# Performance work log

Measured on AMD Instinct MI355X. Metric: run time of the kernel, lower is better.

Reference implementation:

```python
import jax, jax.numpy as jnp
from jax import lax
import numpy as np

NUM_KIND = 4
V, H, B = 34, 32, 4096   # raw vertical (2 rows dropped), horizontal, batch
KS = 33                  # odd-rounded max(V-2, H)
NUM_DEPTH = 4
N_SQ = 100


def _conv(x, w):
    # x: (N,1,h,w), w: (1,1,KS,KS); torch Conv2d == cross-correlation == lax default
    return lax.conv_general_dilated(x, w, (1, 1), 'SAME',
                                    dimension_numbers=('NCHW', 'OIHW', 'NCHW'))


def _conv_k(x, w):
    # x: (K,B,1,h,w) -> conv each map with the shared 1-channel kernel
    k, b, c, h, wd = x.shape
    return _conv(x.reshape(k * b, c, h, wd), w).reshape(k, b, c, h, wd)


def setup_inputs() -> dict:
    key = jax.random.key(0)
    ks = jax.random.split(key, 8)
    std = 0.3
    return {
        'dots':    jax.random.randint(ks[0], (V, H, B), 0, NUM_KIND + 1, dtype=jnp.int32),
        'w_each':  jax.random.normal(ks[1], (1, 1, KS, KS), jnp.float32) * std,
        'w_not':   jax.random.normal(ks[2], (1, 1, KS, KS), jnp.float32) * std,
        'w_not2':  jax.random.normal(ks[3], (1, 1, KS, KS), jnp.float32) * std,
        'w_empty': jax.random.normal(ks[4], (1, 1, KS, KS), jnp.float32) * std,
        'W1':      jax.random.normal(ks[5], (N_SQ, (V - 2) * H), jnp.float32) * std,
        'W2':      jax.random.normal(ks[6], (N_SQ, N_SQ), jnp.float32) * std,
        'W3':      jax.random.normal(ks[7], (1, N_SQ), jnp.float32) * std,
    }


def reference(dots, w_each, w_not, w_not2, w_empty, W1, W2, W3):
    # drop last 2 vertical rows, layout (V-2,H,B) -> (B,1,V-2,H)
    board = dots[:-2].astype(jnp.float32).transpose(2, 0, 1)[:, None]  # (B,1,h,w)

    empty = (board == 0).astype(jnp.float32)
    E = _conv(empty, w_empty)                                           # (B,1,h,w)

    kinds = jnp.arange(1, NUM_KIND + 1, dtype=board.dtype).reshape(NUM_KIND, 1, 1, 1, 1)
    each = (board[None] == kinds).astype(jnp.float32)                   # (K,B,1,h,w)
    notm = ((each + empty[None]) == 0).astype(jnp.float32)              # (K,B,1,h,w)

    # first pass: per-color value, masked to that color's cells
    notm_conv = _conv_k(notm, w_not)      # note: the torch code LOGS the convolved not-mask
    v = _conv_k(each, w_each) + E[None] - notm_conv
    L = each * v                          # each_color_value_log (masked)
    s = jax.nn.sigmoid(L.sum(axis=0))     # all_color_value_2nd, (B,1,h,w)

    # iterative diffusion; torch mutates the log in-place each depth:
    # L <- mask * (L + E + conv2nd(notm_conv * before)); before is detached
    for _ in range(NUM_DEPTH):
        before = lax.stop_gradient(s)
        C = _conv_k(notm_conv * before[None], w_not2)
        L = each * (L + E[None] + C)
        s = jax.nn.sigmoid(L.sum(axis=0))

    feat = s.reshape(s.shape[0], -1)      # (B, (V-2)*H)
    x = jax.nn.leaky_relu(feat @ W1.T, 0.2)
    x = jax.nn.leaky_relu(x @ W2.T, 0.2)
    return x @ W3.T                        # (B,1)
```

## Files before the change

### kernel.cpp

```cpp
#include <hip/hip_runtime.h>
#include <cstdint>
#include <cstddef>


typedef _Float16 f16;
typedef __attribute__((ext_vector_type(8))) _Float16 f16x8;
typedef __attribute__((ext_vector_type(4))) float f32x4;

#define NB   4096
#define PIX  1024
#define MR   (NB * 4)

__device__ __forceinline__ void gld_lds16(const void* g, void* l) {
    __builtin_amdgcn_global_load_lds(
        (const __attribute__((address_space(1))) void*)g,
        (__attribute__((address_space(3))) void*)l, 16, 0, 0);
}

__global__ void build_mats(const float* __restrict__ we, const float* __restrict__ wn,
                           const float* __restrict__ wn2, const float* __restrict__ wem,
                           f16* __restrict__ Mn, f16* __restrict__ Mn2,
                           f16* __restrict__ Mem, f16* __restrict__ Bst) {
    int idx = blockIdx.x * 256 + threadIdx.x;
    int o = idx >> 10, in = idx & 1023;
    int i = o >> 5, j = o & 31, a = in >> 5, b = in & 31;
    int u = a - i + 16, v = b - j + 16;
    bool ok = (u >= 0) && (u < 33) && (v >= 0) && (v < 33);
    int w = u * 33 + v;
    float ve = 0.f, vn = 0.f, vn2 = 0.f, vem = 0.f;
    if (ok) { ve = we[w]; vn = wn[w]; vn2 = wn2[w]; vem = wem[w]; }
    Mn[idx]  = (f16)vn;
    Mn2[idx] = (f16)vn2;
    Mem[idx] = (f16)vem;
    Bst[(size_t)o * 2048 + in]        = (f16)(ve + vn);
    Bst[(size_t)o * 2048 + 1024 + in] = (f16)(vem + vn);
}

__global__ void tn_build(const f16* __restrict__ Mn, float* __restrict__ tn) {
    int o = blockIdx.x * 256 + threadIdx.x;
    float s = 0.f;
    for (int j = 0; j < 128; j++) {
        f16x8 v = *(const f16x8*)(Mn + (size_t)o * 1024 + j * 8);
#pragma unroll
        for (int e = 0; e < 8; e++) s += (float)v[e];
    }
    tn[o] = s;
}

__global__ void build_w1(const float* __restrict__ W1, f16* __restrict__ W1b) {
    int idx = blockIdx.x * 256 + threadIdx.x;
    int j = idx >> 10, i = idx & 1023;
    W1b[idx] = (f16)(j < 100 ? W1[j * 1024 + i] : 0.f);
}

__global__ void build_board(const int* __restrict__ dots, unsigned char* __restrict__ board) {
    __shared__ unsigned char tile[64][68];
    int t = threadIdx.x;
    int bp = blockIdx.x & 15, bn = blockIdx.x >> 4;
    int p0 = bp * 64, n0 = bn * 64;
    int ln = t & 63, lp = t >> 6;
#pragma unroll
    for (int j = 0; j < 16; j++) {
        int p = lp * 16 + j;
        tile[p][ln] = (unsigned char)dots[(size_t)(p0 + p) * 4096 + n0 + ln];
    }
    __syncthreads();
#pragma unroll
    for (int j = 0; j < 16; j++) {
        int n = lp * 16 + j;
        board[(size_t)(n0 + n) * 1024 + p0 + ln] = tile[ln][n];
    }
}

template <int MODE, int ASRC>
__device__ __forceinline__ void run_gemm(
    int bjob, int ypx, int nx, char* smem,
    const f16* __restrict__ X, const f16* __restrict__ B, int K,
    const unsigned char* __restrict__ board, const f16* __restrict__ NCs,
    const f16* __restrict__ Sin, const f16* __restrict__ En,
    const float* __restrict__ tn, float* __restrict__ Lsel,
    f16* __restrict__ outB, int ldo, float* __restrict__ outF) {
    char* smB = smem;
    char* smA = smem + 16384;
    char* smS = smem + 32768;

    const int tid = threadIdx.x;
    const int wv = tid >> 6, ln = tid & 63;
    const int wm = wv >> 1, wn_ = wv & 1;
    const int lr = ln & 15, lq = ln >> 4;

    int xcd = bjob & 7, slot = bjob >> 3;
    int bx = slot % nx;
    int by = xcd * ypx + slot / nx;
    const int rtile = by * 128, otile = bx * 128;
    const int img0 = (ASRC == 4) ? rtile : (rtile >> 2);

    const f32x4 fz = {0.f, 0.f, 0.f, 0.f};
    f32x4 acc[4][4];
#pragma unroll
    for (int i = 0; i < 4; i++)
#pragma unroll
        for (int j = 0; j < 4; j++) acc[i][j] = fz;

    for (int kb = 0; kb < K; kb += 64) {
#pragma unroll
        for (int t = 0; t < 4; t++) {
            int c = t * 256 + wv * 64 + ln;
            int row = c >> 3, gcol = (c & 7) ^ (row & 7);
            gld_lds16(B + (size_t)(otile + row) * K + kb + gcol * 8, smB + c * 16);
        }
        if (ASRC == 0) {
#pragma unroll
            for (int t = 0; t < 4; t++) {
                int c = t * 256 + wv * 64 + ln;
                int row = c >> 3, gcol = (c & 7) ^ (row & 7);
                gld_lds16(X + (size_t)(rtile + row) * K + kb + gcol * 8, smA + c * 16);
            }
        } else if (ASRC == 1) {
#pragma unroll
            for (int t = 0; t < 4; t++) {
                int c = t * 256 + wv * 64 + ln;
                int row = c >> 3, gcol = (c & 7) ^ (row & 7);
                gld_lds16(NCs + (size_t)(rtile + row) * 1024 + kb + gcol * 8, smA + c * 16);
            }
            {
                int c = wv * 64 + ln;
                int row = c >> 3, gcol = (c & 7) ^ (row & 7);
                gld_lds16(Sin + (size_t)(img0 + row) * 1024 + kb + gcol * 8, smS + c * 16);
            }
        } else if (ASRC == 4) {
            int cb = kb;
#pragma unroll
            for (int t = 0; t < 2; t++) {
                int c = t * 256 + wv * 64 + ln;
                int row = c >> 2, g = (c & 3) ^ (row & 3);
                gld_lds16(board + (size_t)(img0 + row) * 1024 + cb + g * 16, smA + c * 16);
            }
        } else {
            int cb = (ASRC == 5) ? (kb & 1023) : kb;
            if (wv < 2) {
                int c = wv * 64 + ln;
                int row = c >> 2, g = (c & 3) ^ (row & 3);
                gld_lds16(board + (size_t)(img0 + row) * 1024 + cb + g * 16, smA + c * 16);
            }
        }
        __syncthreads();

#pragma unroll
        for (int kk = 0; kk < 2; kk++) {
            const int oct = kk * 4 + lq;
            f16x8 af[4], bfr[4];
#pragma unroll
            for (int i = 0; i < 4; i++) {
                int rrow = wm * 64 + i * 16 + lr;
                if (ASRC == 0) {
                    af[i] = *(const f16x8*)(smA + rrow * 128 + (oct ^ (rrow & 7)) * 16);
                } else if (ASRC == 1) {
                    f16x8 nc = *(const f16x8*)(smA + rrow * 128 + (oct ^ (rrow & 7)) * 16);
                    int img = rrow >> 2;
                    f16x8 sv = *(const f16x8*)(smS + img * 128 + (oct ^ (img & 7)) * 16);
                    af[i] = nc * sv;
                } else {
                    int m = (ASRC == 4) ? rrow : (rrow >> 2);
                    int k1 = (rrow & 3) + 1;
                    uint64_t bb = *(const uint64_t*)(smA + m * 64 +
                                    (((oct >> 1)) ^ (m & 3)) * 16 + (oct & 1) * 8);
                    bool ext = (ASRC == 5) && (kb >= 1024);
                    f16x8 v;
#pragma unroll
                    for (int jj = 0; jj < 8; jj++) {
                        int bj = (int)((bb >> (8 * jj)) & 0xff);
                        bool on = (ASRC == 4) ? (bj == 0)
                                : (ASRC == 3) ? (bj != 0 && bj != k1)
                                : ext          ? (bj == 0)
                                               : (bj == k1);
                        v[jj] = on ? (f16)1.f : (f16)0.f;
                    }
                    af[i] = v;
                }
            }
#pragma unroll
            for (int j = 0; j < 4; j++) {
                int brow = wn_ * 64 + j * 16 + lr;
                bfr[j] = *(const f16x8*)(smB + brow * 128 + (oct ^ (brow & 7)) * 16);
            }
#pragma unroll
            for (int i = 0; i < 4; i++)
#pragma unroll
                for (int j = 0; j < 4; j++)
                    acc[i][j] = __builtin_amdgcn_mfma_f32_16x16x32_f16(
                        af[i], bfr[j], acc[i][j], 0, 0, 0);
        }
        __syncthreads();
    }

#pragma unroll
    for (int i = 0; i < 4; i++) {
        int rbase = rtile + wm * 64 + i * 16 + lq * 4;
#pragma unroll
        for (int j = 0; j < 4; j++) {
            int o = otile + wn_ * 64 + j * 16 + lr;
            f32x4 a = acc[i][j];
            if (MODE == 0) {
#pragma unroll
                for (int v = 0; v < 4; v++)
                    outB[(size_t)(rbase + v) * ldo + o] = (f16)a[v];
            } else if (MODE == 5) {
#pragma unroll
                for (int v = 0; v < 4; v++) {
                    float x = a[v];
                    outF[(size_t)(rbase + v) * ldo + o] = x > 0.f ? x : 0.2f * x;
                }
            } else {
                int n = rbase >> 2;
                size_t no = (size_t)n * PIX + o;
                int c = board[no];
                float asel = (c == 1) ? a[0] : (c == 2) ? a[1] : (c == 3) ? a[2] : a[3];
                float Lnew;
                if (MODE == 2) {
                    Lnew = (c > 0) ? (asel - tn[o]) : 0.f;
                } else {
                    float E = (float)En[no];
                    Lnew = (c > 0) ? (Lsel[no] + E + asel) : 0.f;
                }
                float s = 1.f / (1.f + __expf(-Lnew));
                if (MODE != 4) Lsel[no] = Lnew;
                outB[no] = (f16)s;
            }
        }
    }
}

__global__ void __launch_bounds__(256, 4) gemm_fa(
    const f16* __restrict__ Bst, const f16* __restrict__ Mn,
    const f16* __restrict__ Mem, const unsigned char* __restrict__ board,
    const float* __restrict__ tn, float* __restrict__ Lsel,
    f16* __restrict__ Sa, f16* __restrict__ NC, f16* __restrict__ En) {
    __shared__ __attribute__((aligned(16))) char smem[24576];
    int bi = blockIdx.x;
    if (bi < 1024) {
        run_gemm<2, 5>(bi, 16, 8, smem, nullptr, Bst, 2048, board, nullptr,
                       nullptr, nullptr, tn, Lsel, Sa, 0, nullptr);
    } else if (bi < 2048) {
        run_gemm<0, 3>(bi - 1024, 16, 8, smem, nullptr, Mn, 1024, board, nullptr,
                       nullptr, nullptr, nullptr, nullptr, NC, PIX, nullptr);
    } else {
        run_gemm<0, 4>(bi - 2048, 4, 8, smem, nullptr, Mem, 1024, board, nullptr,
                       nullptr, nullptr, nullptr, nullptr, En, PIX, nullptr);
    }
}

template <int MODE>
__global__ void __launch_bounds__(256, 4) gemm_depth(
    const f16* __restrict__ Mn2, const unsigned char* __restrict__ board,
    const f16* __restrict__ NCs, const f16* __restrict__ Sin,
    const f16* __restrict__ En, float* __restrict__ Lsel,
    f16* __restrict__ outB) {
    __shared__ __attribute__((aligned(16))) char smem[36864];
    run_gemm<MODE, 1>(blockIdx.x, 16, 8, smem, nullptr, Mn2, 1024, board, NCs,
                      Sin, En, nullptr, Lsel, outB, 0, nullptr);
}

__global__ void __launch_bounds__(256, 4) gemm_mlp(
    const f16* __restrict__ feat, const f16* __restrict__ W1b,
    float* __restrict__ X1) {
    __shared__ __attribute__((aligned(16))) char smem[32768];
    run_gemm<5, 0>(blockIdx.x, 4, 1, smem, feat, W1b, 1024, nullptr, nullptr,
                   nullptr, nullptr, nullptr, nullptr, nullptr, 128, X1);
}

__global__ void __launch_bounds__(256) mlp23(const float* __restrict__ X1,
                                             const float* __restrict__ W2,
                                             const float* __restrict__ W3,
                                             float* __restrict__ out) {
    __shared__ float sW2[10000];
    __shared__ float sW3[100];
    __shared__ float red[256];
    int t = threadIdx.x;
    for (int idx = t; idx < 10000; idx += 256) sW2[idx] = W2[idx];
    if (t < 100) sW3[t] = W3[t];
    __syncthreads();
    int nb = t >> 2, q = t & 3;
    int n = blockIdx.x * 64 + nb;
    const float* x1 = X1 + (size_t)n * 128;
    float xr[100];
#pragma unroll
    for (int i = 0; i < 100; i++) xr[i] = x1[i];
    float partial = 0.f;
    for (int jj = 0; jj < 25; jj++) {
        int j = q + jj * 4;
        const float* w2r = sW2 + j * 100;
        float acc2 = 0.f;
#pragma unroll
        for (int i = 0; i < 100; i++) acc2 += w2r[i] * xr[i];
        partial += sW3[j] * (acc2 > 0.f ? acc2 : 0.2f * acc2);
    }
    red[t] = partial;
    __syncthreads();
    if (q == 0) out[n] = red[t] + red[t + 1] + red[t + 2] + red[t + 3];
}

extern "C" void kernel_launch(void* const* d_in, const int* in_sizes, int n_in,
                              void* d_out, int out_size, void* d_ws, size_t ws_size,
                              hipStream_t stream) {
    (void)in_sizes; (void)n_in; (void)out_size; (void)ws_size;
    const int*   dots   = (const int*)d_in[0];
    const float* w_each = (const float*)d_in[1];
    const float* w_not  = (const float*)d_in[2];
    const float* w_not2 = (const float*)d_in[3];
    const float* w_emp  = (const float*)d_in[4];
    const float* W1 = (const float*)d_in[5];
    const float* W2 = (const float*)d_in[6];
    const float* W3 = (const float*)d_in[7];
    float* out = (float*)d_out;

    char* ws = (char*)d_ws;
    size_t off = 0;
    auto alloc = [&](size_t bytes) -> char* {
        char* p = ws + off;
        off += (bytes + 255) & ~(size_t)255;
        return p;
    };
    f16* Mn   = (f16*)alloc((size_t)PIX * PIX * 2);
    f16* Mn2  = (f16*)alloc((size_t)PIX * PIX * 2);
    f16* Mem  = (f16*)alloc((size_t)PIX * PIX * 2);
    f16* Bst  = (f16*)alloc((size_t)PIX * 2048 * 2);
    f16* W1b  = (f16*)alloc((size_t)128 * PIX * 2);
    unsigned char* board = (unsigned char*)alloc((size_t)NB * PIX);
    f16*   NC   = (f16*)alloc((size_t)MR * PIX * 2);
    f16*   En   = (f16*)alloc((size_t)NB * PIX * 2);
    f16*   Sa   = (f16*)alloc((size_t)NB * PIX * 2);
    f16*   Sb   = (f16*)alloc((size_t)NB * PIX * 2);
    f16*   feat = (f16*)alloc((size_t)NB * PIX * 2);
    float* Lsel = (float*)alloc((size_t)NB * PIX * 4);
    float* tn   = (float*)alloc((size_t)PIX * 4);
    float* X1   = (float*)alloc((size_t)NB * 128 * 4);

    build_mats<<<4096, 256, 0, stream>>>(w_each, w_not, w_not2, w_emp, Mn, Mn2, Mem, Bst);
    tn_build<<<4, 256, 0, stream>>>(Mn, tn);
    build_w1<<<512, 256, 0, stream>>>(W1, W1b);
    build_board<<<1024, 256, 0, stream>>>(dots, board);

    dim3 blk(256);
    gemm_fa<<<2304, blk, 0, stream>>>(Bst, Mn, Mem, board, tn, Lsel, Sa, NC, En);
    gemm_depth<3><<<1024, blk, 0, stream>>>(Mn2, board, NC, Sa, En, Lsel, Sb);
    gemm_depth<3><<<1024, blk, 0, stream>>>(Mn2, board, NC, Sb, En, Lsel, Sa);
    gemm_depth<3><<<1024, blk, 0, stream>>>(Mn2, board, NC, Sa, En, Lsel, Sb);
    gemm_depth<4><<<1024, blk, 0, stream>>>(Mn2, board, NC, Sb, En, Lsel, feat);
    gemm_mlp<<<32, blk, 0, stream>>>(feat, W1b, X1);
    mlp23<<<64, blk, 0, stream>>>(X1, W2, W3, out);
}
```

Measured before the change: 433.1 us.

## Precompute f16 mask matrices, widen GEMM N-tile to 256, split first-pass GEMMs

A new kernel materializes the per-kind, not-mask and empty-mask indicator matrices in f16 up front, so the GEMMs load them directly instead of decoding board bytes into masks inside the inner loop. The first-pass stacked GEMM (K=2048) is split into separate K=1024 GEMMs: the E and E-plus-not-conv products are stacked along N, and the sigmoid/Lsel init moves into a new elementwise kernel. GEMM tiles become 128x256 with 3 blocks per CU, halving the depth-grid size and reusing each A tile across more outputs. The cost is several large extra mask buffers, more global traffic for the materialized masks, and an extra elementwise pass.

```diff
diff --git a/kernel.cpp b/kernel.cpp
--- a/kernel.cpp
+++ b/kernel.cpp
@@ -20,7 +20,7 @@
 __global__ void build_mats(const float* __restrict__ we, const float* __restrict__ wn,
                            const float* __restrict__ wn2, const float* __restrict__ wem,
                            f16* __restrict__ Mn, f16* __restrict__ Mn2,
-                           f16* __restrict__ Mem, f16* __restrict__ Bst) {
+                           f16* __restrict__ BstS1, f16* __restrict__ BstE) {
     int idx = blockIdx.x * 256 + threadIdx.x;
     int o = idx >> 10, in = idx & 1023;
     int i = o >> 5, j = o & 31, a = in >> 5, b = in & 31;
@@ -29,11 +29,11 @@
     int w = u * 33 + v;
     float ve = 0.f, vn = 0.f, vn2 = 0.f, vem = 0.f;
     if (ok) { ve = we[w]; vn = wn[w]; vn2 = wn2[w]; vem = wem[w]; }
-    Mn[idx]  = (f16)vn;
-    Mn2[idx] = (f16)vn2;
-    Mem[idx] = (f16)vem;
-    Bst[(size_t)o * 2048 + in]        = (f16)(ve + vn);
-    Bst[(size_t)o * 2048 + 1024 + in] = (f16)(vem + vn);
+    Mn[idx]    = (f16)vn;
+    Mn2[idx]   = (f16)vn2;
+    BstS1[idx] = (f16)(ve + vn);
+    BstE[idx]                          = (f16)vem;
+    BstE[(size_t)(1024 + o) * 1024 + in] = (f16)(vem + vn);
 }
 
 __global__ void tn_build(const f16* __restrict__ Mn, float* __restrict__ tn) {
@@ -72,17 +72,43 @@
     }
 }
 
-template <int MODE, int ASRC>
+__global__ void build_masks(const unsigned char* __restrict__ board,
+                            f16* __restrict__ Xe, f16* __restrict__ Xn,
+                            f16* __restrict__ Xz) {
+    int idx = blockIdx.x * 256 + threadIdx.x;
+    int n = idx >> 10, p = idx & 1023;
+    int c = board[idx];
+    Xz[idx] = (f16)(c == 0 ? 1.f : 0.f);
+    size_t base = (size_t)n * 4096 + p;
+#pragma unroll
+    for (int k = 0; k < 4; k++) {
+        Xe[base + k * 1024] = (f16)((c == k + 1) ? 1.f : 0.f);
+        Xn[base + k * 1024] = (f16)((c != 0 && c != k + 1) ? 1.f : 0.f);
+    }
+}
+
+__global__ void mk_sa(const f16* __restrict__ S1sel, const f16* __restrict__ EplusM,
+                      const unsigned char* __restrict__ board,
+                      float* __restrict__ Lsel, f16* __restrict__ Sa) {
+    int idx = blockIdx.x * 256 + threadIdx.x;
+    int c = board[idx];
+    float L = (c > 0) ? ((float)S1sel[idx] + (float)EplusM[idx]) : 0.f;
+    Lsel[idx] = L;
+    Sa[idx] = (f16)(1.f / (1.f + __expf(-L)));
+}
+
+template <int MODE, int ASRC, int NTJ>
 __device__ __forceinline__ void run_gemm(
     int bjob, int ypx, int nx, char* smem,
-    const f16* __restrict__ X, const f16* __restrict__ B, int K,
+    const f16* __restrict__ X, const f16* __restrict__ B,
     const unsigned char* __restrict__ board, const f16* __restrict__ NCs,
     const f16* __restrict__ Sin, const f16* __restrict__ En,
     const float* __restrict__ tn, float* __restrict__ Lsel,
     f16* __restrict__ outB, int ldo, float* __restrict__ outF) {
+    constexpr int BN = NTJ * 32;
     char* smB = smem;
-    char* smA = smem + 16384;
-    char* smS = smem + 32768;
+    char* smA = smem + BN * 128;
+    char* smS = smA + 16384;
 
     const int tid = threadIdx.x;
     const int wv = tid >> 6, ln = tid & 63;
@@ -92,104 +118,62 @@
     int xcd = bjob & 7, slot = bjob >> 3;
     int bx = slot % nx;
     int by = xcd * ypx + slot / nx;
-    const int rtile = by * 128, otile = bx * 128;
-    const int img0 = (ASRC == 4) ? rtile : (rtile >> 2);
+    const int rtile = by * 128, otile = bx * BN;
+    const int img0 = rtile >> 2;
 
     const f32x4 fz = {0.f, 0.f, 0.f, 0.f};
-    f32x4 acc[4][4];
+    f32x4 acc[4][NTJ];
 #pragma unroll
     for (int i = 0; i < 4; i++)
 #pragma unroll
-        for (int j = 0; j < 4; j++) acc[i][j] = fz;
-
-    for (int kb = 0; kb < K; kb += 64) {
+        for (int j = 0; j < NTJ; j++) acc[i][j] = fz;
+
+    for (int kb = 0; kb < 1024; kb += 64) {
+#pragma unroll
+        for (int t = 0; t < NTJ; t++) {
+            int c = t * 256 + wv * 64 + ln;
+            int row = c >> 3, gcol = (c & 7) ^ (row & 7);
+            gld_lds16(B + (size_t)(otile + row) * 1024 + kb + gcol * 8, smB + c * 16);
+        }
 #pragma unroll
         for (int t = 0; t < 4; t++) {
             int c = t * 256 + wv * 64 + ln;
             int row = c >> 3, gcol = (c & 7) ^ (row & 7);
-            gld_lds16(B + (size_t)(otile + row) * K + kb + gcol * 8, smB + c * 16);
-        }
-        if (ASRC == 0) {
-#pragma unroll
-            for (int t = 0; t < 4; t++) {
-                int c = t * 256 + wv * 64 + ln;
-                int row = c >> 3, gcol = (c & 7) ^ (row & 7);
-                gld_lds16(X + (size_t)(rtile + row) * K + kb + gcol * 8, smA + c * 16);
-            }
-        } else if (ASRC == 1) {
-#pragma unroll
-            for (int t = 0; t < 4; t++) {
-                int c = t * 256 + wv * 64 + ln;
-                int row = c >> 3, gcol = (c & 7) ^ (row & 7);
-                gld_lds16(NCs + (size_t)(rtile + row) * 1024 + kb + gcol * 8, smA + c * 16);
-            }
-            {
-                int c = wv * 64 + ln;
-                int row = c >> 3, gcol = (c & 7) ^ (row & 7);
-                gld_lds16(Sin + (size_t)(img0 + row) * 1024 + kb + gcol * 8, smS + c * 16);
-            }
-        } else if (ASRC == 4) {
-            int cb = kb;
-#pragma unroll
-            for (int t = 0; t < 2; t++) {
-                int c = t * 256 + wv * 64 + ln;
-                int row = c >> 2, g = (c & 3) ^ (row & 3);
-                gld_lds16(board + (size_t)(img0 + row) * 1024 + cb + g * 16, smA + c * 16);
-            }
-        } else {
-            int cb = (ASRC == 5) ? (kb & 1023) : kb;
-            if (wv < 2) {
-                int c = wv * 64 + ln;
-                int row = c >> 2, g = (c & 3) ^ (row & 3);
-                gld_lds16(board + (size_t)(img0 + row) * 1024 + cb + g * 16, smA + c * 16);
-            }
+            const f16* src = (ASRC == 0) ? X : NCs;
+            gld_lds16(src + (size_t)(rtile + row) * 1024 + kb + gcol * 8, smA + c * 16);
+        }
+        if (ASRC == 1) {
+            int c = wv * 64 + ln;
+            int row = c >> 3, gcol = (c & 7) ^ (row & 7);
+            gld_lds16(Sin + (size_t)(img0 + row) * 1024 + kb + gcol * 8, smS + c * 16);
         }
         __syncthreads();
 
 #pragma unroll
         for (int kk = 0; kk < 2; kk++) {
             const int oct = kk * 4 + lq;
-            f16x8 af[4], bfr[4];
+            f16x8 af[4];
 #pragma unroll
             for (int i = 0; i < 4; i++) {
                 int rrow = wm * 64 + i * 16 + lr;
                 if (ASRC == 0) {
                     af[i] = *(const f16x8*)(smA + rrow * 128 + (oct ^ (rrow & 7)) * 16);
-                } else if (ASRC == 1) {
+                } else {
                     f16x8 nc = *(const f16x8*)(smA + rrow * 128 + (oct ^ (rrow & 7)) * 16);
                     int img = rrow >> 2;
                     f16x8 sv = *(const f16x8*)(smS + img * 128 + (oct ^ (img & 7)) * 16);
                     af[i] = nc * sv;
-                } else {
-                    int m = (ASRC == 4) ? rrow : (rrow >> 2);
-                    int k1 = (rrow & 3) + 1;
-                    uint64_t bb = *(const uint64_t*)(smA + m * 64 +
-                                    (((oct >> 1)) ^ (m & 3)) * 16 + (oct & 1) * 8);
-                    bool ext = (ASRC == 5) && (kb >= 1024);
-                    f16x8 v;
-#pragma unroll
-                    for (int jj = 0; jj < 8; jj++) {
-                        int bj = (int)((bb >> (8 * jj)) & 0xff);
-                        bool on = (ASRC == 4) ? (bj == 0)
-                                : (ASRC == 3) ? (bj != 0 && bj != k1)
-                                : ext          ? (bj == 0)
-                                               : (bj == k1);
-                        v[jj] = on ? (f16)1.f : (f16)0.f;
-                    }
-                    af[i] = v;
                 }
             }
 #pragma unroll
-            for (int j = 0; j < 4; j++) {
-                int brow = wn_ * 64 + j * 16 + lr;
-                bfr[j] = *(const f16x8*)(smB + brow * 128 + (oct ^ (brow & 7)) * 16);
+            for (int j = 0; j < NTJ; j++) {
+                int brow = wn_ * (NTJ * 16) + j * 16 + lr;
+                f16x8 bf = *(const f16x8*)(smB + brow * 128 + (oct ^ (brow & 7)) * 16);
+#pragma unroll
+                for (int i = 0; i < 4; i++)
+                    acc[i][j] = __builtin_amdgcn_mfma_f32_16x16x32_f16(
+                        af[i], bf, acc[i][j], 0, 0, 0);
             }
-#pragma unroll
-            for (int i = 0; i < 4; i++)
-#pragma unroll
-                for (int j = 0; j < 4; j++)
-                    acc[i][j] = __builtin_amdgcn_mfma_f32_16x16x32_f16(
-                        af[i], bfr[j], acc[i][j], 0, 0, 0);
         }
         __syncthreads();
     }
@@ -198,13 +182,23 @@
     for (int i = 0; i < 4; i++) {
         int rbase = rtile + wm * 64 + i * 16 + lq * 4;
 #pragma unroll
-        for (int j = 0; j < 4; j++) {
-            int o = otile + wn_ * 64 + j * 16 + lr;
+        for (int j = 0; j < NTJ; j++) {
+            int o = otile + wn_ * (NTJ * 16) + j * 16 + lr;
             f32x4 a = acc[i][j];
             if (MODE == 0) {
 #pragma unroll
                 for (int v = 0; v < 4; v++)
                     outB[(size_t)(rbase + v) * ldo + o] = (f16)a[v];
+            } else if (MODE == 2) {
+#pragma unroll
+                for (int v = 0; v < 4; v++) {
+                    int n = rbase + v;
+                    if (o < 1024)
+                        outB[(size_t)n * 1024 + o] = (f16)a[v];
+                    else
+                        outB[(size_t)(NB + n) * 1024 + (o - 1024)] =
+                            (f16)(a[v] - tn[o - 1024]);
+                }
             } else if (MODE == 5) {
 #pragma unroll
                 for (int v = 0; v < 4; v++) {
@@ -216,57 +210,57 @@
                 size_t no = (size_t)n * PIX + o;
                 int c = board[no];
                 float asel = (c == 1) ? a[0] : (c == 2) ? a[1] : (c == 3) ? a[2] : a[3];
-                float Lnew;
-                if (MODE == 2) {
-                    Lnew = (c > 0) ? (asel - tn[o]) : 0.f;
+                if (MODE == 1) {
+                    outB[no] = (f16)asel;
                 } else {
                     float E = (float)En[no];
-                    Lnew = (c > 0) ? (Lsel[no] + E + asel) : 0.f;
+                    float Lnew = (c > 0) ? (Lsel[no] + E + asel) : 0.f;
+                    float s = 1.f / (1.f + __expf(-Lnew));
+                    if (MODE != 4) Lsel[no] = Lnew;
+                    outB[no] = (f16)s;
                 }
-                float s = 1.f / (1.f + __expf(-Lnew));
-                if (MODE != 4) Lsel[no] = Lnew;
-                outB[no] = (f16)s;
             }
         }
     }
 }
 
-__global__ void __launch_bounds__(256, 4) gemm_fa(
-    const f16* __restrict__ Bst, const f16* __restrict__ Mn,
-    const f16* __restrict__ Mem, const unsigned char* __restrict__ board,
-    const float* __restrict__ tn, float* __restrict__ Lsel,
-    f16* __restrict__ Sa, f16* __restrict__ NC, f16* __restrict__ En) {
-    __shared__ __attribute__((aligned(16))) char smem[24576];
+__global__ void __launch_bounds__(256, 3) gemm_fa(
+    const f16* __restrict__ Xe, const f16* __restrict__ Xn,
+    const f16* __restrict__ Xz, const f16* __restrict__ BstS1,
+    const f16* __restrict__ Mn, const f16* __restrict__ BstE,
+    const unsigned char* __restrict__ board, const float* __restrict__ tn,
+    f16* __restrict__ S1sel, f16* __restrict__ NC, f16* __restrict__ EnBoth) {
+    __shared__ __attribute__((aligned(16))) char smem[49152];
     int bi = blockIdx.x;
-    if (bi < 1024) {
-        run_gemm<2, 5>(bi, 16, 8, smem, nullptr, Bst, 2048, board, nullptr,
-                       nullptr, nullptr, tn, Lsel, Sa, 0, nullptr);
-    } else if (bi < 2048) {
-        run_gemm<0, 3>(bi - 1024, 16, 8, smem, nullptr, Mn, 1024, board, nullptr,
-                       nullptr, nullptr, nullptr, nullptr, NC, PIX, nullptr);
+    if (bi < 512) {
+        run_gemm<1, 0, 8>(bi, 16, 4, smem, Xe, BstS1, board, nullptr, nullptr,
+                          nullptr, nullptr, nullptr, S1sel, 0, nullptr);
+    } else if (bi < 1024) {
+        run_gemm<0, 0, 8>(bi - 512, 16, 4, smem, Xn, Mn, nullptr, nullptr, nullptr,
+                          nullptr, nullptr, nullptr, NC, PIX, nullptr);
     } else {
-        run_gemm<0, 4>(bi - 2048, 4, 8, smem, nullptr, Mem, 1024, board, nullptr,
-                       nullptr, nullptr, nullptr, nullptr, En, PIX, nullptr);
+        run_gemm<2, 0, 8>(bi - 1024, 4, 8, smem, Xz, BstE, nullptr, nullptr, nullptr,
+                          nullptr, tn, nullptr, EnBoth, 0, nullptr);
     }
 }
 
 template <int MODE>
-__global__ void __launch_bounds__(256, 4) gemm_depth(
+__global__ void __launch_bounds__(256, 3) gemm_depth(
     const f16* __restrict__ Mn2, const unsigned char* __restrict__ board,
     const f16* __restrict__ NCs, const f16* __restrict__ Sin,
     const f16* __restrict__ En, float* __restrict__ Lsel,
     f16* __restrict__ outB) {
-    __shared__ __attribute__((aligned(16))) char smem[36864];
-    run_gemm<MODE, 1>(blockIdx.x, 16, 8, smem, nullptr, Mn2, 1024, board, NCs,
-                      Sin, En, nullptr, Lsel, outB, 0, nullptr);
-}
-
-__global__ void __launch_bounds__(256, 4) gemm_mlp(
+    __shared__ __attribute__((aligned(16))) char smem[53248];
+    run_gemm<MODE, 1, 8>(blockIdx.x, 16, 4, smem, nullptr, Mn2, board, NCs,
+                         Sin, En, nullptr, Lsel, outB, 0, nullptr);
+}
+
+__global__ void __launch_bounds__(256, 3) gemm_mlp(
     const f16* __restrict__ feat, const f16* __restrict__ W1b,
     float* __restrict__ X1) {
     __shared__ __attribute__((aligned(16))) char smem[32768];
-    run_gemm<5, 0>(blockIdx.x, 4, 1, smem, feat, W1b, 1024, nullptr, nullptr,
-                   nullptr, nullptr, nullptr, nullptr, nullptr, 128, X1);
+    run_gemm<5, 0, 4>(blockIdx.x, 4, 1, smem, feat, W1b, nullptr, nullptr,
+                      nullptr, nullptr, nullptr, nullptr, nullptr, 128, X1);
 }
 
 __global__ void __launch_bounds__(256) mlp23(const float* __restrict__ X1,
@@ -321,32 +315,42 @@
         off += (bytes + 255) & ~(size_t)255;
         return p;
     };
-    f16* Mn   = (f16*)alloc((size_t)PIX * PIX * 2);
-    f16* Mn2  = (f16*)alloc((size_t)PIX * PIX * 2);
-    f16* Mem  = (f16*)alloc((size_t)PIX * PIX * 2);
-    f16* Bst  = (f16*)alloc((size_t)PIX * 2048 * 2);
-    f16* W1b  = (f16*)alloc((size_t)128 * PIX * 2);
+    f16* Mn    = (f16*)alloc((size_t)PIX * PIX * 2);
+    f16* Mn2   = (f16*)alloc((size_t)PIX * PIX * 2);
+    f16* BstS1 = (f16*)alloc((size_t)PIX * PIX * 2);
+    f16* BstE  = (f16*)alloc((size_t)2048 * PIX * 2);
+    f16* W1b   = (f16*)alloc((size_t)128 * PIX * 2);
     unsigned char* board = (unsigned char*)alloc((size_t)NB * PIX);
-    f16*   NC   = (f16*)alloc((size_t)MR * PIX * 2);
-    f16*   En   = (f16*)alloc((size_t)NB * PIX * 2);
-    f16*   Sa   = (f16*)alloc((size_t)NB * PIX * 2);
-    f16*   Sb   = (f16*)alloc((size_t)NB * PIX * 2);
-    f16*   feat = (f16*)alloc((size_t)NB * PIX * 2);
-    float* Lsel = (float*)alloc((size_t)NB * PIX * 4);
-    float* tn   = (float*)alloc((size_t)PIX * 4);
-    float* X1   = (float*)alloc((size_t)NB * 128 * 4);
-
-    build_mats<<<4096, 256, 0, stream>>>(w_each, w_not, w_not2, w_emp, Mn, Mn2, Mem, Bst);
+    f16* Xe    = (f16*)alloc((size_t)MR * PIX * 2);
+    f16* Xn    = (f16*)alloc((size_t)MR * PIX * 2);
+    f16* Xz    = (f16*)alloc((size_t)NB * PIX * 2);
+    f16* NC    = (f16*)alloc((size_t)MR * PIX * 2);
+    f16* EnBoth= (f16*)alloc((size_t)2 * NB * PIX * 2);
+    f16* S1sel = (f16*)alloc((size_t)NB * PIX * 2);
+    f16* Sa    = (f16*)alloc((size_t)NB * PIX * 2);
+    f16* Sb    = (f16*)alloc((size_t)NB * PIX * 2);
+    f16* feat  = (f16*)alloc((size_t)NB * PIX * 2);
+    float* Lsel= (float*)alloc((size_t)NB * PIX * 4);
+    float* tn  = (float*)alloc((size_t)PIX * 4);
+    float* X1  = (float*)alloc((size_t)NB * 128 * 4);
+
+    build_board<<<1024, 256, 0, stream>>>(dots, board);
+    build_mats<<<4096, 256, 0, stream>>>(w_each, w_not, w_not2, w_emp,
+                                         Mn, Mn2, BstS1, BstE);
     tn_build<<<4, 256, 0, stream>>>(Mn, tn);
     build_w1<<<512, 256, 0, stream>>>(W1, W1b);
-    build_board<<<1024, 256, 0, stream>>>(dots, board);
+    build_masks<<<16384, 256, 0, stream>>>(board, Xe, Xn, Xz);
 
     dim3 blk(256);
-    gemm_fa<<<2304, blk, 0, stream>>>(Bst, Mn, Mem, board, tn, Lsel, Sa, NC, En);
-    gemm_depth<3><<<1024, blk, 0, stream>>>(Mn2, board, NC, Sa, En, Lsel, Sb);
-    gemm_depth<3><<<1024, blk, 0, stream>>>(Mn2, board, NC, Sb, En, Lsel, Sa);
-    gemm_depth<3><<<1024, blk, 0, stream>>>(Mn2, board, NC, Sa, En, Lsel, Sb);
-    gemm_depth<4><<<1024, blk, 0, stream>>>(Mn2, board, NC, Sb, En, Lsel, feat);
+    gemm_fa<<<1280, blk, 0, stream>>>(Xe, Xn, Xz, BstS1, Mn, BstE, board, tn,
+                                      S1sel, NC, EnBoth);
+    f16* En = EnBoth;
+    f16* EplusM = EnBoth + (size_t)NB * PIX;
+    mk_sa<<<16384, blk, 0, stream>>>(S1sel, EplusM, board, Lsel, Sa);
+    gemm_depth<3><<<512, blk, 0, stream>>>(Mn2, board, NC, Sa, En, Lsel, Sb);
+    gemm_depth<3><<<512, blk, 0, stream>>>(Mn2, board, NC, Sb, En, Lsel, Sa);
+    gemm_depth<3><<<512, blk, 0, stream>>>(Mn2, board, NC, Sa, En, Lsel, Sb);
+    gemm_depth<4><<<512, blk, 0, stream>>>(Mn2, board, NC, Sb, En, Lsel, feat);
     gemm_mlp<<<32, blk, 0, stream>>>(feat, W1b, X1);
     mlp23<<<64, blk, 0, stream>>>(X1, W2, W3, out);
 }
```

Result: slower. 755.1 us (+74.3%).

## Split first-pass GEMM, add elementwise sigmoid kernel, prefuse NC*S into LDS

Applied to the files above, without the earlier changes.

Replaces the stacked K=2048 first-pass GEMM (each+not and empty+not weights, with a tn correction) by a plain K=1024 GEMM on Me. A new elementwise kernel then combines the result with the already computed En and NC to form L and the first sigmoid. The depth GEMMs now multiply NC by S in registers before writing to LDS, instead of staging S separately and multiplying after each LDS read. The LDS load mapping is also reordered per wave. This removes K work and the tn kernel, but adds an extra launch and an extra full pass over NC, En and L, and it drops async global-to-LDS loads for the depth A operand.

```diff
diff --git a/kernel.cpp b/kernel.cpp
--- a/kernel.cpp
+++ b/kernel.cpp
@@ -19,8 +19,8 @@
 
 __global__ void build_mats(const float* __restrict__ we, const float* __restrict__ wn,
                            const float* __restrict__ wn2, const float* __restrict__ wem,
-                           f16* __restrict__ Mn, f16* __restrict__ Mn2,
-                           f16* __restrict__ Mem, f16* __restrict__ Bst) {
+                           f16* __restrict__ Me, f16* __restrict__ Mn,
+                           f16* __restrict__ Mn2, f16* __restrict__ Mem) {
     int idx = blockIdx.x * 256 + threadIdx.x;
     int o = idx >> 10, in = idx & 1023;
     int i = o >> 5, j = o & 31, a = in >> 5, b = in & 31;
@@ -29,22 +29,10 @@
     int w = u * 33 + v;
     float ve = 0.f, vn = 0.f, vn2 = 0.f, vem = 0.f;
     if (ok) { ve = we[w]; vn = wn[w]; vn2 = wn2[w]; vem = wem[w]; }
+    Me[idx]  = (f16)ve;
     Mn[idx]  = (f16)vn;
     Mn2[idx] = (f16)vn2;
     Mem[idx] = (f16)vem;
-    Bst[(size_t)o * 2048 + in]        = (f16)(ve + vn);
-    Bst[(size_t)o * 2048 + 1024 + in] = (f16)(vem + vn);
-}
-
-__global__ void tn_build(const f16* __restrict__ Mn, float* __restrict__ tn) {
-    int o = blockIdx.x * 256 + threadIdx.x;
-    float s = 0.f;
-    for (int j = 0; j < 128; j++) {
-        f16x8 v = *(const f16x8*)(Mn + (size_t)o * 1024 + j * 8);
-#pragma unroll
-        for (int e = 0; e < 8; e++) s += (float)v[e];
-    }
-    tn[o] = s;
 }
 
 __global__ void build_w1(const float* __restrict__ W1, f16* __restrict__ W1b) {
@@ -72,17 +60,32 @@
     }
 }
 
+__global__ void mk_sa(const f16* __restrict__ S1sel, const f16* __restrict__ En,
+                      const f16* __restrict__ NC,
+                      const unsigned char* __restrict__ board,
+                      float* __restrict__ Lsel, f16* __restrict__ Sa) {
+    int idx = blockIdx.x * 256 + threadIdx.x;
+    int n = idx >> 10, o = idx & 1023;
+    int c = board[idx];
+    float L = 0.f;
+    if (c > 0) {
+        float ncsel = (float)NC[(size_t)(4 * n + c - 1) * 1024 + o];
+        L = (float)S1sel[idx] + (float)En[idx] - ncsel;
+    }
+    Lsel[idx] = L;
+    Sa[idx] = (f16)(1.f / (1.f + __expf(-L)));
+}
+
 template <int MODE, int ASRC>
 __device__ __forceinline__ void run_gemm(
     int bjob, int ypx, int nx, char* smem,
-    const f16* __restrict__ X, const f16* __restrict__ B, int K,
+    const f16* __restrict__ X, const f16* __restrict__ B,
     const unsigned char* __restrict__ board, const f16* __restrict__ NCs,
     const f16* __restrict__ Sin, const f16* __restrict__ En,
-    const float* __restrict__ tn, float* __restrict__ Lsel,
-    f16* __restrict__ outB, int ldo, float* __restrict__ outF) {
+    float* __restrict__ Lsel, f16* __restrict__ outB, int ldo,
+    float* __restrict__ outF) {
     char* smB = smem;
     char* smA = smem + 16384;
-    char* smS = smem + 32768;
 
     const int tid = threadIdx.x;
     const int wv = tid >> 6, ln = tid & 63;
@@ -102,46 +105,42 @@
 #pragma unroll
         for (int j = 0; j < 4; j++) acc[i][j] = fz;
 
-    for (int kb = 0; kb < K; kb += 64) {
+    for (int kb = 0; kb < 1024; kb += 64) {
 #pragma unroll
         for (int t = 0; t < 4; t++) {
-            int c = t * 256 + wv * 64 + ln;
+            int c = (wv * 4 + t) * 64 + ln;
             int row = c >> 3, gcol = (c & 7) ^ (row & 7);
-            gld_lds16(B + (size_t)(otile + row) * K + kb + gcol * 8, smB + c * 16);
+            gld_lds16(B + (size_t)(otile + row) * 1024 + kb + gcol * 8, smB + c * 16);
         }
         if (ASRC == 0) {
 #pragma unroll
             for (int t = 0; t < 4; t++) {
-                int c = t * 256 + wv * 64 + ln;
+                int c = (wv * 4 + t) * 64 + ln;
                 int row = c >> 3, gcol = (c & 7) ^ (row & 7);
-                gld_lds16(X + (size_t)(rtile + row) * K + kb + gcol * 8, smA + c * 16);
+                gld_lds16(X + (size_t)(rtile + row) * 1024 + kb + gcol * 8, smA + c * 16);
             }
         } else if (ASRC == 1) {
 #pragma unroll
             for (int t = 0; t < 4; t++) {
-                int c = t * 256 + wv * 64 + ln;
+                int c = (wv * 4 + t) * 64 + ln;
                 int row = c >> 3, gcol = (c & 7) ^ (row & 7);
-                gld_lds16(NCs + (size_t)(rtile + row) * 1024 + kb + gcol * 8, smA + c * 16);
-            }
-            {
-                int c = wv * 64 + ln;
-                int row = c >> 3, gcol = (c & 7) ^ (row & 7);
-                gld_lds16(Sin + (size_t)(img0 + row) * 1024 + kb + gcol * 8, smS + c * 16);
+                int gr = rtile + row;
+                f16x8 nc = *(const f16x8*)(NCs + (size_t)gr * 1024 + kb + gcol * 8);
+                f16x8 sv = *(const f16x8*)(Sin + (size_t)(gr >> 2) * 1024 + kb + gcol * 8);
+                *(f16x8*)(smA + c * 16) = nc * sv;
             }
         } else if (ASRC == 4) {
-            int cb = kb;
 #pragma unroll
             for (int t = 0; t < 2; t++) {
                 int c = t * 256 + wv * 64 + ln;
                 int row = c >> 2, g = (c & 3) ^ (row & 3);
-                gld_lds16(board + (size_t)(img0 + row) * 1024 + cb + g * 16, smA + c * 16);
+                gld_lds16(board + (size_t)(img0 + row) * 1024 + kb + g * 16, smA + c * 16);
             }
         } else {
-            int cb = (ASRC == 5) ? (kb & 1023) : kb;
             if (wv < 2) {
                 int c = wv * 64 + ln;
                 int row = c >> 2, g = (c & 3) ^ (row & 3);
-                gld_lds16(board + (size_t)(img0 + row) * 1024 + cb + g * 16, smA + c * 16);
+                gld_lds16(board + (size_t)(img0 + row) * 1024 + kb + g * 16, smA + c * 16);
             }
         }
         __syncthreads();
@@ -153,27 +152,20 @@
 #pragma unroll
             for (int i = 0; i < 4; i++) {
                 int rrow = wm * 64 + i * 16 + lr;
-                if (ASRC == 0) {
+                if (ASRC == 0 || ASRC == 1) {
                     af[i] = *(const f16x8*)(smA + rrow * 128 + (oct ^ (rrow & 7)) * 16);
-                } else if (ASRC == 1) {
-                    f16x8 nc = *(const f16x8*)(smA + rrow * 128 + (oct ^ (rrow & 7)) * 16);
-                    int img = rrow >> 2;
-                    f16x8 sv = *(const f16x8*)(smS + img * 128 + (oct ^ (img & 7)) * 16);
-                    af[i] = nc * sv;
                 } else {
                     int m = (ASRC == 4) ? rrow : (rrow >> 2);
                     int k1 = (rrow & 3) + 1;
                     uint64_t bb = *(const uint64_t*)(smA + m * 64 +
-                                    (((oct >> 1)) ^ (m & 3)) * 16 + (oct & 1) * 8);
-                    bool ext = (ASRC == 5) && (kb >= 1024);
+                                    ((oct >> 1) ^ (m & 3)) * 16 + (oct & 1) * 8);
                     f16x8 v;
 #pragma unroll
                     for (int jj = 0; jj < 8; jj++) {
                         int bj = (int)((bb >> (8 * jj)) & 0xff);
-                        bool on = (ASRC == 4) ? (bj == 0)
+                        bool on = (ASRC == 2) ? (bj == k1)
                                 : (ASRC == 3) ? (bj != 0 && bj != k1)
-                                : ext          ? (bj == 0)
-                                               : (bj == k1);
+                                              : (bj == 0);
                         v[jj] = on ? (f16)1.f : (f16)0.f;
                     }
                     af[i] = v;
@@ -216,37 +208,35 @@
                 size_t no = (size_t)n * PIX + o;
                 int c = board[no];
                 float asel = (c == 1) ? a[0] : (c == 2) ? a[1] : (c == 3) ? a[2] : a[3];
-                float Lnew;
-                if (MODE == 2) {
-                    Lnew = (c > 0) ? (asel - tn[o]) : 0.f;
+                if (MODE == 1) {
+                    outB[no] = (f16)asel;
                 } else {
                     float E = (float)En[no];
-                    Lnew = (c > 0) ? (Lsel[no] + E + asel) : 0.f;
+                    float Lnew = (c > 0) ? (Lsel[no] + E + asel) : 0.f;
+                    float s = 1.f / (1.f + __expf(-Lnew));
+                    if (MODE != 4) Lsel[no] = Lnew;
+                    outB[no] = (f16)s;
                 }
-                float s = 1.f / (1.f + __expf(-Lnew));
-                if (MODE != 4) Lsel[no] = Lnew;
-                outB[no] = (f16)s;
             }
         }
     }
 }
 
 __global__ void __launch_bounds__(256, 4) gemm_fa(
-    const f16* __restrict__ Bst, const f16* __restrict__ Mn,
+    const f16* __restrict__ Me, const f16* __restrict__ Mn,
     const f16* __restrict__ Mem, const unsigned char* __restrict__ board,
-    const float* __restrict__ tn, float* __restrict__ Lsel,
-    f16* __restrict__ Sa, f16* __restrict__ NC, f16* __restrict__ En) {
+    f16* __restrict__ S1sel, f16* __restrict__ NC, f16* __restrict__ En) {
     __shared__ __attribute__((aligned(16))) char smem[24576];
     int bi = blockIdx.x;
     if (bi < 1024) {
-        run_gemm<2, 5>(bi, 16, 8, smem, nullptr, Bst, 2048, board, nullptr,
-                       nullptr, nullptr, tn, Lsel, Sa, 0, nullptr);
+        run_gemm<1, 2>(bi, 16, 8, smem, nullptr, Me, board, nullptr, nullptr,
+                       nullptr, nullptr, S1sel, 0, nullptr);
     } else if (bi < 2048) {
-        run_gemm<0, 3>(bi - 1024, 16, 8, smem, nullptr, Mn, 1024, board, nullptr,
-                       nullptr, nullptr, nullptr, nullptr, NC, PIX, nullptr);
+        run_gemm<0, 3>(bi - 1024, 16, 8, smem, nullptr, Mn, board, nullptr, nullptr,
+                       nullptr, nullptr, NC, PIX, nullptr);
     } else {
-        run_gemm<0, 4>(bi - 2048, 4, 8, smem, nullptr, Mem, 1024, board, nullptr,
-                       nullptr, nullptr, nullptr, nullptr, En, PIX, nullptr);
+        run_gemm<0, 4>(bi - 2048, 4, 8, smem, nullptr, Mem, board, nullptr, nullptr,
+                       nullptr, nullptr, En, PIX, nullptr);
     }
 }
 
@@ -256,17 +246,17 @@
     const f16* __restrict__ NCs, const f16* __restrict__ Sin,
     const f16* __restrict__ En, float* __restrict__ Lsel,
     f16* __restrict__ outB) {
-    __shared__ __attribute__((aligned(16))) char smem[36864];
-    run_gemm<MODE, 1>(blockIdx.x, 16, 8, smem, nullptr, Mn2, 1024, board, NCs,
-                      Sin, En, nullptr, Lsel, outB, 0, nullptr);
+    __shared__ __attribute__((aligned(16))) char smem[32768];
+    run_gemm<MODE, 1>(blockIdx.x, 16, 8, smem, nullptr, Mn2, board, NCs,
+                      Sin, En, Lsel, outB, 0, nullptr);
 }
 
 __global__ void __launch_bounds__(256, 4) gemm_mlp(
     const f16* __restrict__ feat, const f16* __restrict__ W1b,
     float* __restrict__ X1) {
     __shared__ __attribute__((aligned(16))) char smem[32768];
-    run_gemm<5, 0>(blockIdx.x, 4, 1, smem, feat, W1b, 1024, nullptr, nullptr,
-                   nullptr, nullptr, nullptr, nullptr, nullptr, 128, X1);
+    run_gemm<5, 0>(blockIdx.x, 4, 1, smem, feat, W1b, nullptr, nullptr,
+                   nullptr, nullptr, nullptr, nullptr, 128, X1);
 }
 
 __global__ void __launch_bounds__(256) mlp23(const float* __restrict__ X1,
@@ -321,28 +311,29 @@
         off += (bytes + 255) & ~(size_t)255;
         return p;
     };
-    f16* Mn   = (f16*)alloc((size_t)PIX * PIX * 2);
-    f16* Mn2  = (f16*)alloc((size_t)PIX * PIX * 2);
-    f16* Mem  = (f16*)alloc((size_t)PIX * PIX * 2);
-    f16* Bst  = (f16*)alloc((size_t)PIX * 2048 * 2);
-    f16* W1b  = (f16*)alloc((size_t)128 * PIX * 2);
+    f16* Me    = (f16*)alloc((size_t)PIX * PIX * 2);
+    f16* Mn    = (f16*)alloc((size_t)PIX * PIX * 2);
+    f16* Mn2   = (f16*)alloc((size_t)PIX * PIX * 2);
+    f16* Mem   = (f16*)alloc((size_t)PIX * PIX * 2);
+    f16* W1b   = (f16*)alloc((size_t)128 * PIX * 2);
     unsigned char* board = (unsigned char*)alloc((size_t)NB * PIX);
-    f16*   NC   = (f16*)alloc((size_t)MR * PIX * 2);
-    f16*   En   = (f16*)alloc((size_t)NB * PIX * 2);
-    f16*   Sa   = (f16*)alloc((size_t)NB * PIX * 2);
-    f16*   Sb   = (f16*)alloc((size_t)NB * PIX * 2);
-    f16*   feat = (f16*)alloc((size_t)NB * PIX * 2);
-    float* Lsel = (float*)alloc((size_t)NB * PIX * 4);
-    float* tn   = (float*)alloc((size_t)PIX * 4);
-    float* X1   = (float*)alloc((size_t)NB * 128 * 4);
-
-    build_mats<<<4096, 256, 0, stream>>>(w_each, w_not, w_not2, w_emp, Mn, Mn2, Mem, Bst);
-    tn_build<<<4, 256, 0, stream>>>(Mn, tn);
+    f16* NC    = (f16*)alloc((size_t)MR * PIX * 2);
+    f16* En    = (f16*)alloc((size_t)NB * PIX * 2);
+    f16* S1sel = (f16*)alloc((size_t)NB * PIX * 2);
+    f16* Sa    = (f16*)alloc((size_t)NB * PIX * 2);
+    f16* Sb    = (f16*)alloc((size_t)NB * PIX * 2);
+    f16* feat  = (f16*)alloc((size_t)NB * PIX * 2);
+    float* Lsel= (float*)alloc((size_t)NB * PIX * 4);
+    float* X1  = (float*)alloc((size_t)NB * 128 * 4);
+
+    build_board<<<1024, 256, 0, stream>>>(dots, board);
+    build_mats<<<4096, 256, 0, stream>>>(w_each, w_not, w_not2, w_emp,
+                                         Me, Mn, Mn2, Mem);
     build_w1<<<512, 256, 0, stream>>>(W1, W1b);
-    build_board<<<1024, 256, 0, stream>>>(dots, board);
 
     dim3 blk(256);
-    gemm_fa<<<2304, blk, 0, stream>>>(Bst, Mn, Mem, board, tn, Lsel, Sa, NC, En);
+    gemm_fa<<<2304, blk, 0, stream>>>(Me, Mn, Mem, board, S1sel, NC, En);
+    mk_sa<<<16384, blk, 0, stream>>>(S1sel, En, NC, board, Lsel, Sa);
     gemm_depth<3><<<1024, blk, 0, stream>>>(Mn2, board, NC, Sa, En, Lsel, Sb);
     gemm_depth<3><<<1024, blk, 0, stream>>>(Mn2, board, NC, Sb, En, Lsel, Sa);
     gemm_depth<3><<<1024, blk, 0, stream>>>(Mn2, board, NC, Sa, En, Lsel, Sb);
```

Result: no change. 428.2 us (-1.1%).
